# Kernel optimization log

Hardware: AMD Instinct MI355X
Metric: run time of the kernel (lower is better)

Reference implementation:

```python
import jax, jax.numpy as jnp
import numpy as np

B, T, C, HS = 16, 2048, 2048, 256  # batch, seq (=BLOCK_SIZE), N_EMBD, head_size


def setup_inputs() -> dict:
    key = jax.random.key(0)
    k0, k1, k2, k3 = jax.random.split(key, 4)
    token_embd = jax.random.normal(k0, (B, T, C), dtype=jnp.float32)
    # nn.Linear(C, HS, bias=False); store as [C, HS] so projection is x @ W
    scale = 1.0 / np.sqrt(C)
    Wk = jax.random.normal(k1, (C, HS), dtype=jnp.float32) * scale
    Wq = jax.random.normal(k2, (C, HS), dtype=jnp.float32) * scale
    Wv = jax.random.normal(k3, (C, HS), dtype=jnp.float32) * scale
    return {"token_embd": token_embd, "Wk": Wk, "Wq": Wq, "Wv": Wv}


def reference(token_embd, Wk, Wq, Wv):
    Bc, Tc, Cc = token_embd.shape
    k = token_embd @ Wk  # [B,T,HS]
    q = token_embd @ Wq  # [B,T,HS]
    v = token_embd @ Wv  # [B,T,HS]
    # NOTE faithful quirks of the source: k @ q^T (not q @ k^T) and
    # MULTIPLY by sqrt(C) where C = N_EMBD.
    weights = jnp.einsum("bih,bjh->bij", k, q) * (Cc ** 0.5)  # [B,T,T]
    # causal mask: tril==0 (upper triangle, j>i) -> -inf
    i = jnp.arange(Tc)[:, None]
    j = jnp.arange(Tc)[None, :]
    weights = jnp.where(j > i, -jnp.inf, weights)
    # softmax over dim=1 (rows / first T axis), as in the source
    weights = jax.nn.softmax(weights, axis=1)
    # dropout p=0.0 / eval mode -> identity
    output = jnp.einsum("bij,bjh->bih", weights, v)  # [B,T,HS]
    return output
```

## Files before the change

kernel.cpp:

```cpp
#include <hip/hip_runtime.h>
#include <math.h>

#define Bn 16
#define Tn 2048
#define Cn 2048
#define HSn 256
#define SCALE 45.254833995939045f
#define NEG_BIG (-1e30f)
#define NT 16
#define NPAIR 136
#define WN 524288

typedef __attribute__((ext_vector_type(8))) short bf16x8;
typedef __attribute__((ext_vector_type(4))) float f32x4;
typedef unsigned short u16;
typedef unsigned int u32;

__device__ __forceinline__ u16 bf16_rn(float f) {
    u32 u = __float_as_uint(f);
    u += 0x7fffu + ((u >> 16) & 1u);
    return (u16)(u >> 16);
}
__device__ __forceinline__ float bf16_rn_f(float f) {
    return __uint_as_float((u32)bf16_rn(f) << 16);
}

#define GLOAD_LDS16(gp, lp)                                                      \
    __builtin_amdgcn_global_load_lds(                                            \
        (const __attribute__((address_space(1))) unsigned int*)(gp),             \
        (__attribute__((address_space(3))) unsigned int*)(lp), 16, 0, 0)

#define WAITV0_LG0 asm volatile("s_waitcnt vmcnt(0) lgkmcnt(0)" ::: "memory")
#define WAITV2_LG0 asm volatile("s_waitcnt vmcnt(2) lgkmcnt(0)" ::: "memory")
#define WAITLG0    asm volatile("s_waitcnt lgkmcnt(0)" ::: "memory")
#define BARRIER    __builtin_amdgcn_s_barrier()

__global__ __launch_bounds__(256) void split_w_kernel(
    const float* __restrict__ Wk, const float* __restrict__ Wq,
    const float* __restrict__ Wv, u16* __restrict__ Wt)
{
    const int n = threadIdx.x, k = blockIdx.x, mat = blockIdx.y;
    const float* src = (mat == 0) ? Wk : (mat == 1) ? Wq : Wv;
    const float f = src[(long)k * HSn + n];
    const u32 u = __float_as_uint(f);
    const u16 hb = (u16)(u >> 16);
    const float fh = __uint_as_float(u & 0xffff0000u);
    const u16 lb = bf16_rn(f - fh);
    u16* base = Wt + (long)mat * 2 * WN;
    base[(long)n * Cn + k] = hb;
    base[WN + (long)n * Cn + k] = lb;
}

__global__ __launch_bounds__(512, 2) void projm_fused_kernel(
    const float* __restrict__ X, const u16* __restrict__ Wt,
    u16* __restrict__ Khi, u16* __restrict__ Klo,
    u16* __restrict__ Qhi, u16* __restrict__ Qlo, u16* __restrict__ VbfT)
{
    __shared__ u16 Ahi[4096], Alo[4096];
    __shared__ u16 Bbuf[20480];

    const int tid = threadIdx.x, l = tid & 63, w = tid >> 6;
    const int wm = w & 3, wn = w >> 2;
    const int m0 = blockIdx.x * 128, n0 = blockIdx.y * 128;

    int xoff[2], aoff[2];
    #pragma unroll
    for (int p = 0; p < 2; ++p) {
        const int idx4 = p * 512 + tid;
        const int row  = idx4 >> 3;
        const int kk4  = (idx4 & 7) * 4;
        xoff[p] = (m0 + row) * Cn + kk4;
        aoff[p] = (row >> 4) * 512 + (((row & 15) | ((kk4 >> 3) << 4)) * 8) + (kk4 & 7);
    }

    int wgoff[5];
    const int lbase = w * 5 * 512;
    #pragma unroll
    for (int j = 0; j < 5; ++j) {
        const int g    = w * 5 + j;
        const int half = g >> 3;
        const int cc   = g & 7;
        const int nrow = n0 + cc * 16 + (l & 15);
        wgoff[j] = half * WN + nrow * Cn + ((l >> 4) << 3);
    }

    f32x4 accK[2][4], accQ[2][4], accV[2][4];
    #pragma unroll
    for (int mt = 0; mt < 2; ++mt)
        #pragma unroll
        for (int nt = 0; nt < 4; ++nt)
            #pragma unroll
            for (int r = 0; r < 4; ++r) {
                accK[mt][nt][r] = 0.f; accQ[mt][nt][r] = 0.f; accV[mt][nt][r] = 0.f;
            }

    float4 xA[2], xB[2];

    auto convert_write = [&](const float4 (&xr)[2]) {
        #pragma unroll
        for (int p = 0; p < 2; ++p) {
            const float xf[4] = {xr[p].x, xr[p].y, xr[p].z, xr[p].w};
            ushort4 h4, l4;
            #pragma unroll
            for (int c = 0; c < 4; ++c) {
                const u32 u = __float_as_uint(xf[c]);
                ((u16*)&h4)[c] = (u16)(u >> 16);
                const float fh = __uint_as_float(u & 0xffff0000u);
                ((u16*)&l4)[c] = bf16_rn(xf[c] - fh);
            }
            *(ushort4*)(Ahi + aoff[p]) = h4;
            *(ushort4*)(Alo + aoff[p]) = l4;
        }
    };

    auto mfma_all = [&]() {
        bf16x8 ah[2], al[2];
        #pragma unroll
        for (int mt = 0; mt < 2; ++mt) {
            ah[mt] = *(const bf16x8*)(Ahi + (wm * 2 + mt) * 512 + l * 8);
            al[mt] = *(const bf16x8*)(Alo + (wm * 2 + mt) * 512 + l * 8);
        }
        {
            bf16x8 bh[4], bl[4];
            #pragma unroll
            for (int nt = 0; nt < 4; ++nt) {
                bh[nt] = *(const bf16x8*)(Bbuf + (0 * 8 + wn * 4 + nt) * 512 + l * 8);
                bl[nt] = *(const bf16x8*)(Bbuf + (1 * 8 + wn * 4 + nt) * 512 + l * 8);
            }
            #pragma unroll
            for (int mt = 0; mt < 2; ++mt)
                #pragma unroll
                for (int nt = 0; nt < 4; ++nt) {
                    accK[mt][nt] = __builtin_amdgcn_mfma_f32_16x16x32_bf16(ah[mt], bh[nt], accK[mt][nt], 0, 0, 0);
                    accK[mt][nt] = __builtin_amdgcn_mfma_f32_16x16x32_bf16(ah[mt], bl[nt], accK[mt][nt], 0, 0, 0);
                    accK[mt][nt] = __builtin_amdgcn_mfma_f32_16x16x32_bf16(al[mt], bh[nt], accK[mt][nt], 0, 0, 0);
                }
        }
        {
            bf16x8 bh[4], bl[4];
            #pragma unroll
            for (int nt = 0; nt < 4; ++nt) {
                bh[nt] = *(const bf16x8*)(Bbuf + (2 * 8 + wn * 4 + nt) * 512 + l * 8);
                bl[nt] = *(const bf16x8*)(Bbuf + (3 * 8 + wn * 4 + nt) * 512 + l * 8);
            }
            #pragma unroll
            for (int mt = 0; mt < 2; ++mt)
                #pragma unroll
                for (int nt = 0; nt < 4; ++nt) {
                    accQ[mt][nt] = __builtin_amdgcn_mfma_f32_16x16x32_bf16(ah[mt], bh[nt], accQ[mt][nt], 0, 0, 0);
                    accQ[mt][nt] = __builtin_amdgcn_mfma_f32_16x16x32_bf16(ah[mt], bl[nt], accQ[mt][nt], 0, 0, 0);
                    accQ[mt][nt] = __builtin_amdgcn_mfma_f32_16x16x32_bf16(al[mt], bh[nt], accQ[mt][nt], 0, 0, 0);
                }
        }
        {
            bf16x8 bh[4];
            #pragma unroll
            for (int nt = 0; nt < 4; ++nt)
                bh[nt] = *(const bf16x8*)(Bbuf + (4 * 8 + wn * 4 + nt) * 512 + l * 8);
            #pragma unroll
            for (int mt = 0; mt < 2; ++mt)
                #pragma unroll
                for (int nt = 0; nt < 4; ++nt)
                    accV[mt][nt] = __builtin_amdgcn_mfma_f32_16x16x32_bf16(ah[mt], bh[nt], accV[mt][nt], 0, 0, 0);
        }
    };

    xA[0] = *(const float4*)(X + xoff[0]);
    xA[1] = *(const float4*)(X + xoff[1]);

    #pragma unroll 1
    for (int k0 = 0; k0 < Cn; k0 += 64) {
        #pragma unroll
        for (int j = 0; j < 5; ++j)
            GLOAD_LDS16(Wt + wgoff[j] + k0, Bbuf + lbase + j * 512);
        __builtin_amdgcn_sched_barrier(0);
        xB[0] = *(const float4*)(X + xoff[0] + k0 + 32);
        xB[1] = *(const float4*)(X + xoff[1] + k0 + 32);
        convert_write(xA);
        WAITV2_LG0;
        BARRIER;
        mfma_all();
        WAITLG0;
        BARRIER;
        #pragma unroll
        for (int j = 0; j < 5; ++j)
            GLOAD_LDS16(Wt + wgoff[j] + k0 + 32, Bbuf + lbase + j * 512);
        __builtin_amdgcn_sched_barrier(0);
        const int kn = (k0 + 64 < Cn) ? k0 + 64 : 0;
        xA[0] = *(const float4*)(X + xoff[0] + kn);
        xA[1] = *(const float4*)(X + xoff[1] + kn);
        convert_write(xB);
        WAITV2_LG0;
        BARRIER;
        mfma_all();
        WAITLG0;
        BARRIER;
    }

    const int quad = (l >> 4) * 4, col = l & 15;
    u16* Vlds = Bbuf;
    #pragma unroll
    for (int mt = 0; mt < 2; ++mt)
        #pragma unroll
        for (int nt = 0; nt < 4; ++nt)
            #pragma unroll
            for (int r = 0; r < 4; ++r) {
                const long i = m0 + wm * 32 + mt * 16 + quad + r;
                const int  j = n0 + wn * 64 + nt * 16 + col;
                {
                    const float f = accK[mt][nt][r];
                    const u32 u = __float_as_uint(f);
                    Khi[i * HSn + j] = (u16)(u >> 16);
                    const float fh = __uint_as_float(u & 0xffff0000u);
                    Klo[i * HSn + j] = bf16_rn(f - fh);
                }
                {
                    const float f = accQ[mt][nt][r];
                    const u32 u = __float_as_uint(f);
                    Qhi[i * HSn + j] = (u16)(u >> 16);
                    const float fh = __uint_as_float(u & 0xffff0000u);
                    Qlo[i * HSn + j] = bf16_rn(f - fh);
                }
                Vlds[(wm * 32 + mt * 16 + quad + r) * 128 + wn * 64 + nt * 16 + col]
                    = bf16_rn(accV[mt][nt][r]);
            }
    __syncthreads();
    {
        const int bidx = m0 >> 11, jb = m0 & (Tn - 1);
        #pragma unroll
        for (int hh = 0; hh < 4; ++hh) {
            const int hl = hh * 32 + (tid >> 4);
            const int h  = n0 + hl;
            const int jl = (tid & 15) * 8;
            union { uint4 v; u16 s[8]; } pk;
            #pragma unroll
            for (int e = 0; e < 8; ++e) pk.s[e] = Vlds[(jl + e) * 128 + hl];
            *(uint4*)(VbfT + ((long)bidx * HSn + h) * Tn + jb + jl) = pk.v;
        }
    }
}

__device__ __forceinline__ void score_tile_mfma(
    const u16* __restrict__ Khi, const u16* __restrict__ Klo,
    const u16* __restrict__ Qhi, const u16* __restrict__ Qlo,
    long base, int i0, int j0,
    u16* Ab0, u16* Bb0, u16* Ab1, u16* Bb1,
    f32x4 (&acc)[4][4], int tid)
{
    const int l = tid & 63, w = tid >> 6;
    const int wm = w & 1, wn = w >> 1;
    const int lrow = l & 15, lk8 = (l >> 4) << 3;

    #pragma unroll
    for (int a = 0; a < 4; ++a)
        #pragma unroll
        for (int bb = 0; bb < 4; ++bb)
            #pragma unroll
            for (int r = 0; r < 4; ++r) acc[a][bb][r] = 0.f;

    const u16* hiP = wn ? Qhi : Khi;
    const u16* loP = wn ? Qlo : Klo;
    const int  t0  = wn ? j0 : i0;
    long rowoff[4];
    #pragma unroll
    for (int m2 = 0; m2 < 4; ++m2) {
        const int mt = (w & 1) * 4 + m2;
        rowoff[m2] = base + (long)(t0 + mt * 16 + lrow) * HSn + lk8;
    }
    u16* dst0 = (wn ? Bb0 : Ab0) + (w & 1) * 8 * 512;
    u16* dst1 = (wn ? Bb1 : Ab1) + (w & 1) * 8 * 512;

    auto stage = [&](int h0, u16* dw) {
        #pragma unroll
        for (int q = 0; q < 8; ++q) {
            const u16* sp = (q & 1) ? loP : hiP;
            GLOAD_LDS16(sp + rowoff[q >> 1] + h0, dw + q * 512);
        }
    };
    auto step = [&](const u16* Ab, const u16* Bb) {
        bf16x8 bh[4], bl[4];
        #pragma unroll
        for (int nt = 0; nt < 4; ++nt) {
            const int c2 = (wn * 4 + nt) * 2;
            bh[nt] = *(const bf16x8*)(Bb + (c2    ) * 512 + l * 8);
            bl[nt] = *(const bf16x8*)(Bb + (c2 + 1) * 512 + l * 8);
        }
        #pragma unroll
        for (int mt = 0; mt < 4; ++mt) {
            const int c2 = (wm * 4 + mt) * 2;
            const bf16x8 ah = *(const bf16x8*)(Ab + (c2    ) * 512 + l * 8);
            const bf16x8 al = *(const bf16x8*)(Ab + (c2 + 1) * 512 + l * 8);
            #pragma unroll
            for (int nt = 0; nt < 4; ++nt) {
                acc[mt][nt] = __builtin_amdgcn_mfma_f32_16x16x32_bf16(ah, bh[nt], acc[mt][nt], 0, 0, 0);
                acc[mt][nt] = __builtin_amdgcn_mfma_f32_16x16x32_bf16(ah, bl[nt], acc[mt][nt], 0, 0, 0);
                acc[mt][nt] = __builtin_amdgcn_mfma_f32_16x16x32_bf16(al, bh[nt], acc[mt][nt], 0, 0, 0);
            }
        }
    };

    stage(0, dst0);
    WAITV0_LG0;
    BARRIER;
    #pragma unroll 1
    for (int ks = 0; ks < 8; ks += 2) {
        stage((ks + 1) * 32, dst1);
        step(Ab0, Bb0);
        WAITV0_LG0;
        BARRIER;
        if (ks + 2 < 8) stage((ks + 2) * 32, dst0);
        step(Ab1, Bb1);
        WAITV0_LG0;
        BARRIER;
    }
}

__device__ __forceinline__ void pair_from_p(int p, int& it, int& jt) {
    it = (int)((sqrtf(8.f * (float)p + 1.f) - 1.f) * 0.5f);
    while ((it + 1) * (it + 2) / 2 <= p) ++it;
    while (it * (it + 1) / 2 > p) --it;
    jt = p - it * (it + 1) / 2;
}

__global__ __launch_bounds__(256) void stats1_kernel(
    const u16* __restrict__ Khi, const u16* __restrict__ Klo,
    const u16* __restrict__ Qhi, const u16* __restrict__ Qlo,
    u16* __restrict__ Pm, u16* __restrict__ Pd)
{
    __shared__ u16 s_lds[32768];
    __shared__ float redm[2][128], redd[2][128];

    const int tid = threadIdx.x, l = tid & 63, w = tid >> 6;
    const int wm = w & 1, wn = w >> 1;
    const int b = blockIdx.y;
    int it, jt; pair_from_p(blockIdx.x, it, jt);
    const long base = (long)b * Tn * HSn;

    f32x4 acc[4][4];
    score_tile_mfma(Khi, Klo, Qhi, Qlo, base, it * 128, jt * 128,
                    s_lds, s_lds + 8192, s_lds + 16384, s_lds + 24576, acc, tid);

    const int rquad = (l >> 4) * 4, col = l & 15;
    #pragma unroll
    for (int nt = 0; nt < 4; ++nt) {
        const int j = jt * 128 + wn * 64 + nt * 16 + col;
        float m = NEG_BIG;
        #pragma unroll
        for (int mt = 0; mt < 4; ++mt)
            #pragma unroll
            for (int r = 0; r < 4; ++r) {
                const int i = it * 128 + wm * 64 + mt * 16 + rquad + r;
                const float sv = (i >= j) ? acc[mt][nt][r] * SCALE : NEG_BIG;
                acc[mt][nt][r] = sv;
                m = fmaxf(m, sv);
            }
        m = fmaxf(m, __shfl_xor(m, 16));
        m = fmaxf(m, __shfl_xor(m, 32));
        float d = 0.f;
        #pragma unroll
        for (int mt = 0; mt < 4; ++mt)
            #pragma unroll
            for (int r = 0; r < 4; ++r)
                d += __expf(acc[mt][nt][r] - m);
        d += __shfl_xor(d, 16);
        d += __shfl_xor(d, 32);
        if (l < 16) {
            redm[wm][wn * 64 + nt * 16 + l] = m;
            redd[wm][wn * 64 + nt * 16 + l] = d;
        }
    }
    __syncthreads();
    if (tid < 128) {
        const float m0 = redm[0][tid], m1 = redm[1][tid];
        const float d0 = redd[0][tid], d1 = redd[1][tid];
        const float M = fmaxf(m0, m1);
        float D = d0 * __expf(m0 - M) + d1 * __expf(m1 - M);
        const float Mb = bf16_rn_f(M);
        D *= __expf(M - Mb);
        const long idx = ((long)b * NPAIR + blockIdx.x) * 128 + tid;
        Pm[idx] = (u16)(__float_as_uint(Mb) >> 16);
        Pd[idx] = bf16_rn(D);
    }
}

__global__ __launch_bounds__(128) void stats2_kernel(
    const u16* __restrict__ Pm, const u16* __restrict__ Pd,
    float* __restrict__ Ms, float* __restrict__ Rd)
{
    const int b = blockIdx.y, jt = blockIdx.x, jl = threadIdx.x;
    float M = NEG_BIG, D = 0.f;
    for (int it = jt; it < NT; ++it) {
        const int p = it * (it + 1) / 2 + jt;
        const long idx = ((long)b * NPAIR + p) * 128 + jl;
        const float m = __uint_as_float((u32)Pm[idx] << 16);
        const float d = __uint_as_float((u32)Pd[idx] << 16);
        const float Mn = fmaxf(M, m);
        D = D * __expf(M - Mn) + d * __expf(m - Mn);
        M = Mn;
    }
    Ms[(long)b * Tn + jt * 128 + jl] = M;
    Rd[(long)b * Tn + jt * 128 + jl] = 1.f / D;
}

__global__ __launch_bounds__(256) void out_kernel(
    const u16* __restrict__ Khi, const u16* __restrict__ Klo,
    const u16* __restrict__ Qhi, const u16* __restrict__ Qlo,
    const u16* __restrict__ VbfT, const float* __restrict__ Ms,
    const float* __restrict__ Rd, float* __restrict__ Out)
{
    __shared__ u16 u_lds[33792];
    u16* Pf    = u_lds;
    u16* Vfrag = u_lds + 17408;

    const int tid = threadIdx.x, l = tid & 63, w = tid >> 6;
    const int wm = w & 1, wn = w >> 1;
    const int lrow = l & 15, lk8 = (l >> 4) << 3;
    const int b = blockIdx.y;
    int it, jt; pair_from_p(blockIdx.x, it, jt);
    const long base = (long)b * Tn * HSn;

    f32x4 acc[4][4];
    score_tile_mfma(Khi, Klo, Qhi, Qlo, base, it * 128, jt * 128,
                    u_lds, u_lds + 8192, u_lds + 16384, u_lds + 24576, acc, tid);

    auto stage_v = [&](int ph) {
        #pragma unroll
        for (int q = 0; q < 8; ++q) {
            const int hh = ph * 128 + q * 16 + lrow;
            const long ga = ((long)b * HSn + hh) * Tn + jt * 128 + w * 32 + lk8;
            GLOAD_LDS16(VbfT + ga, Vfrag + (w * 8 + q) * 512);
        }
    };

    stage_v(0);

    const int rquad = (l >> 4) * 4, col = l & 15;
    float mj[4], rj[4];
    #pragma unroll
    for (int nt = 0; nt < 4; ++nt) {
        const int j = jt * 128 + wn * 64 + nt * 16 + col;
        mj[nt] = Ms[(long)b * Tn + j];
        rj[nt] = Rd[(long)b * Tn + j];
    }
    #pragma unroll
    for (int nt = 0; nt < 4; ++nt) {
        const int j = jt * 128 + wn * 64 + nt * 16 + col;
        #pragma unroll
        for (int mt = 0; mt < 4; ++mt)
            #pragma unroll
            for (int r = 0; r < 4; ++r) {
                const int i = it * 128 + wm * 64 + mt * 16 + rquad + r;
                const float pv = (i >= j)
                    ? __expf(acc[mt][nt][r] * SCALE - mj[nt]) * rj[nt] : 0.f;
                Pf[(wm * 64 + mt * 16 + rquad + r) * 136 + wn * 64 + nt * 16 + col]
                    = bf16_rn(pv);
            }
    }

    auto pv_store = [&](int ph) {
        f32x4 o[4][4];
        #pragma unroll
        for (int a = 0; a < 4; ++a)
            #pragma unroll
            for (int bb = 0; bb < 4; ++bb)
                #pragma unroll
                for (int r = 0; r < 4; ++r) o[a][bb][r] = 0.f;
        #pragma unroll
        for (int kj = 0; kj < 4; ++kj) {
            bf16x8 aP[4];
            #pragma unroll
            for (int mt = 0; mt < 4; ++mt)
                aP[mt] = *(const bf16x8*)(Pf + (wm * 64 + mt * 16 + lrow) * 136 + kj * 32 + lk8);
            #pragma unroll
            for (int nt = 0; nt < 4; ++nt) {
                const bf16x8 bV = *(const bf16x8*)(Vfrag + (kj * 8 + wn * 4 + nt) * 512 + l * 8);
                #pragma unroll
                for (int mt = 0; mt < 4; ++mt)
                    o[mt][nt] = __builtin_amdgcn_mfma_f32_16x16x32_bf16(aP[mt], bV, o[mt][nt], 0, 0, 0);
            }
        }
        #pragma unroll
        for (int mt = 0; mt < 4; ++mt)
            #pragma unroll
            for (int nt = 0; nt < 4; ++nt)
                #pragma unroll
                for (int r = 0; r < 4; ++r) {
                    const int i = it * 128 + wm * 64 + mt * 16 + rquad + r;
                    const int h = ph * 128 + wn * 64 + nt * 16 + col;
                    atomicAdd(&Out[((long)b * Tn + i) * HSn + h], o[mt][nt][r]);
                }
    };

    __syncthreads();
    pv_store(0);
    __syncthreads();
    stage_v(1);
    __syncthreads();
    pv_store(1);
}

extern "C" void kernel_launch(void* const* d_in, const int* in_sizes, int n_in,
                              void* d_out, int out_size, void* d_ws, size_t ws_size,
                              hipStream_t stream) {
    const float* X  = (const float*)d_in[0];
    const float* Wk = (const float*)d_in[1];
    const float* Wq = (const float*)d_in[2];
    const float* Wv = (const float*)d_in[3];

    const long nE = (long)Bn * Tn * HSn;
    u16* Khi = (u16*)d_ws;
    u16* Klo = Khi + nE;
    u16* Qhi = Khi + 2 * nE;
    u16* Qlo = Khi + 3 * nE;
    u16* VbfT = Khi + 4 * nE;
    u16* Wt  = Khi + 5 * nE;
    u16* Pm  = Wt + 6L * WN;
    u16* Pd  = Pm + (long)Bn * NPAIR * 128;
    float* Ms = (float*)(Pd + (long)Bn * NPAIR * 128);
    float* Rd = Ms + (long)Bn * Tn;

    split_w_kernel<<<dim3(Cn, 3), 256, 0, stream>>>(Wk, Wq, Wv, Wt);
    projm_fused_kernel<<<dim3((Bn * Tn) / 128, HSn / 128), 512, 0, stream>>>(
        X, Wt, Khi, Klo, Qhi, Qlo, VbfT);
    stats1_kernel<<<dim3(NPAIR, Bn), 256, 0, stream>>>(Khi, Klo, Qhi, Qlo, Pm, Pd);
    stats2_kernel<<<dim3(NT, Bn), 128, 0, stream>>>(Pm, Pd, Ms, Rd);
    hipMemsetAsync(d_out, 0, (size_t)out_size * sizeof(float), stream);
    out_kernel<<<dim3(NPAIR, Bn), 256, 0, stream>>>(Khi, Klo, Qhi, Qlo, VbfT, Ms, Rd,
                                                    (float*)d_out);
}
```

Baseline: 1.005 ms.

## Double-buffer projection LDS, single-buffer score tile, pipeline V staging in PV

The projection kernel gets ping-pong LDS buffers for the A and B tiles, so the next slice's loads and conversion overlap the current MFMA work and one barrier pair per half-step goes away. The score-tile helper drops its double buffering to a single buffer with a full wait each step, which shrinks LDS use in the stats and PV kernels, presumably to allow more resident blocks. The PV kernel splits the head dimension into four 64-wide phases and issues the next V slice before the atomic stores, so staging overlaps the output writes. The trade-off is less latency hiding in the score GEMM and more LDS use in the projection kernel.

```diff
diff --git a/kernel.cpp b/kernel.cpp
--- a/kernel.cpp
+++ b/kernel.cpp
@@ -30,10 +30,11 @@
         (const __attribute__((address_space(1))) unsigned int*)(gp),             \
         (__attribute__((address_space(3))) unsigned int*)(lp), 16, 0, 0)
 
-#define WAITV0_LG0 asm volatile("s_waitcnt vmcnt(0) lgkmcnt(0)" ::: "memory")
-#define WAITV2_LG0 asm volatile("s_waitcnt vmcnt(2) lgkmcnt(0)" ::: "memory")
-#define WAITLG0    asm volatile("s_waitcnt lgkmcnt(0)" ::: "memory")
-#define BARRIER    __builtin_amdgcn_s_barrier()
+#define WAITV0_LG0  asm volatile("s_waitcnt vmcnt(0) lgkmcnt(0)" ::: "memory")
+#define WAITV2_LG0  asm volatile("s_waitcnt vmcnt(2) lgkmcnt(0)" ::: "memory")
+#define WAITV32_LG0 asm volatile("s_waitcnt vmcnt(32) lgkmcnt(0)" ::: "memory")
+#define WAITLG0     asm volatile("s_waitcnt lgkmcnt(0)" ::: "memory")
+#define BARRIER     __builtin_amdgcn_s_barrier()
 
 __global__ __launch_bounds__(256) void split_w_kernel(
     const float* __restrict__ Wk, const float* __restrict__ Wq,
@@ -56,8 +57,8 @@
     u16* __restrict__ Khi, u16* __restrict__ Klo,
     u16* __restrict__ Qhi, u16* __restrict__ Qlo, u16* __restrict__ VbfT)
 {
-    __shared__ u16 Ahi[4096], Alo[4096];
-    __shared__ u16 Bbuf[20480];
+    __shared__ u16 Ahi0[4096], Alo0[4096], Ahi1[4096], Alo1[4096];
+    __shared__ u16 Bb0[20480], Bb1[20480];
 
     const int tid = threadIdx.x, l = tid & 63, w = tid >> 6;
     const int wm = w & 3, wn = w >> 2;
@@ -96,7 +97,7 @@
 
     float4 xA[2], xB[2];
 
-    auto convert_write = [&](const float4 (&xr)[2]) {
+    auto convert_write = [&](const float4 (&xr)[2], u16* Ah, u16* Al) {
         #pragma unroll
         for (int p = 0; p < 2; ++p) {
             const float xf[4] = {xr[p].x, xr[p].y, xr[p].z, xr[p].w};
@@ -108,24 +109,24 @@
                 const float fh = __uint_as_float(u & 0xffff0000u);
                 ((u16*)&l4)[c] = bf16_rn(xf[c] - fh);
             }
-            *(ushort4*)(Ahi + aoff[p]) = h4;
-            *(ushort4*)(Alo + aoff[p]) = l4;
+            *(ushort4*)(Ah + aoff[p]) = h4;
+            *(ushort4*)(Al + aoff[p]) = l4;
         }
     };
 
-    auto mfma_all = [&]() {
+    auto mfma_all = [&](const u16* Ah, const u16* Al, const u16* Bb) {
         bf16x8 ah[2], al[2];
         #pragma unroll
         for (int mt = 0; mt < 2; ++mt) {
-            ah[mt] = *(const bf16x8*)(Ahi + (wm * 2 + mt) * 512 + l * 8);
-            al[mt] = *(const bf16x8*)(Alo + (wm * 2 + mt) * 512 + l * 8);
+            ah[mt] = *(const bf16x8*)(Ah + (wm * 2 + mt) * 512 + l * 8);
+            al[mt] = *(const bf16x8*)(Al + (wm * 2 + mt) * 512 + l * 8);
         }
         {
             bf16x8 bh[4], bl[4];
             #pragma unroll
             for (int nt = 0; nt < 4; ++nt) {
-                bh[nt] = *(const bf16x8*)(Bbuf + (0 * 8 + wn * 4 + nt) * 512 + l * 8);
-                bl[nt] = *(const bf16x8*)(Bbuf + (1 * 8 + wn * 4 + nt) * 512 + l * 8);
+                bh[nt] = *(const bf16x8*)(Bb + (0 * 8 + wn * 4 + nt) * 512 + l * 8);
+                bl[nt] = *(const bf16x8*)(Bb + (1 * 8 + wn * 4 + nt) * 512 + l * 8);
             }
             #pragma unroll
             for (int mt = 0; mt < 2; ++mt)
@@ -140,8 +141,8 @@
             bf16x8 bh[4], bl[4];
             #pragma unroll
             for (int nt = 0; nt < 4; ++nt) {
-                bh[nt] = *(const bf16x8*)(Bbuf + (2 * 8 + wn * 4 + nt) * 512 + l * 8);
-                bl[nt] = *(const bf16x8*)(Bbuf + (3 * 8 + wn * 4 + nt) * 512 + l * 8);
+                bh[nt] = *(const bf16x8*)(Bb + (2 * 8 + wn * 4 + nt) * 512 + l * 8);
+                bl[nt] = *(const bf16x8*)(Bb + (3 * 8 + wn * 4 + nt) * 512 + l * 8);
             }
             #pragma unroll
             for (int mt = 0; mt < 2; ++mt)
@@ -156,7 +157,7 @@
             bf16x8 bh[4];
             #pragma unroll
             for (int nt = 0; nt < 4; ++nt)
-                bh[nt] = *(const bf16x8*)(Bbuf + (4 * 8 + wn * 4 + nt) * 512 + l * 8);
+                bh[nt] = *(const bf16x8*)(Bb + (4 * 8 + wn * 4 + nt) * 512 + l * 8);
             #pragma unroll
             for (int mt = 0; mt < 2; ++mt)
                 #pragma unroll
@@ -167,38 +168,42 @@
 
     xA[0] = *(const float4*)(X + xoff[0]);
     xA[1] = *(const float4*)(X + xoff[1]);
+    #pragma unroll
+    for (int j = 0; j < 5; ++j)
+        GLOAD_LDS16(Wt + wgoff[j], Bb0 + lbase + j * 512);
+    xB[0] = *(const float4*)(X + xoff[0] + 32);
+    xB[1] = *(const float4*)(X + xoff[1] + 32);
+    convert_write(xA, Ahi0, Alo0);
+    WAITV2_LG0;
+    BARRIER;
 
     #pragma unroll 1
     for (int k0 = 0; k0 < Cn; k0 += 64) {
+        const int kn  = (k0 + 64 < Cn) ? k0 + 64 : 0;
+        const int kn3 = (k0 + 96 < Cn) ? k0 + 96 : 0;
         #pragma unroll
         for (int j = 0; j < 5; ++j)
-            GLOAD_LDS16(Wt + wgoff[j] + k0, Bbuf + lbase + j * 512);
-        __builtin_amdgcn_sched_barrier(0);
-        xB[0] = *(const float4*)(X + xoff[0] + k0 + 32);
-        xB[1] = *(const float4*)(X + xoff[1] + k0 + 32);
-        convert_write(xA);
+            GLOAD_LDS16(Wt + wgoff[j] + k0 + 32, Bb1 + lbase + j * 512);
+        xA[0] = *(const float4*)(X + xoff[0] + kn);
+        xA[1] = *(const float4*)(X + xoff[1] + kn);
+        convert_write(xB, Ahi1, Alo1);
+        mfma_all(Ahi0, Alo0, Bb0);
         WAITV2_LG0;
         BARRIER;
-        mfma_all();
-        WAITLG0;
-        BARRIER;
         #pragma unroll
         for (int j = 0; j < 5; ++j)
-            GLOAD_LDS16(Wt + wgoff[j] + k0 + 32, Bbuf + lbase + j * 512);
-        __builtin_amdgcn_sched_barrier(0);
-        const int kn = (k0 + 64 < Cn) ? k0 + 64 : 0;
-        xA[0] = *(const float4*)(X + xoff[0] + kn);
-        xA[1] = *(const float4*)(X + xoff[1] + kn);
-        convert_write(xB);
+            GLOAD_LDS16(Wt + wgoff[j] + kn, Bb0 + lbase + j * 512);
+        xB[0] = *(const float4*)(X + xoff[0] + kn3);
+        xB[1] = *(const float4*)(X + xoff[1] + kn3);
+        convert_write(xA, Ahi0, Alo0);
+        mfma_all(Ahi1, Alo1, Bb1);
         WAITV2_LG0;
         BARRIER;
-        mfma_all();
-        WAITLG0;
-        BARRIER;
     }
 
     const int quad = (l >> 4) * 4, col = l & 15;
-    u16* Vlds = Bbuf;
+    u16* Vlds = Bb0;
+    __syncthreads();
     #pragma unroll
     for (int mt = 0; mt < 2; ++mt)
         #pragma unroll
@@ -244,7 +249,7 @@
     const u16* __restrict__ Khi, const u16* __restrict__ Klo,
     const u16* __restrict__ Qhi, const u16* __restrict__ Qlo,
     long base, int i0, int j0,
-    u16* Ab0, u16* Bb0, u16* Ab1, u16* Bb1,
+    u16* Ab0, u16* Bb0,
     f32x4 (&acc)[4][4], int tid)
 {
     const int l = tid & 63, w = tid >> 6;
@@ -268,28 +273,29 @@
         rowoff[m2] = base + (long)(t0 + mt * 16 + lrow) * HSn + lk8;
     }
     u16* dst0 = (wn ? Bb0 : Ab0) + (w & 1) * 8 * 512;
-    u16* dst1 = (wn ? Bb1 : Ab1) + (w & 1) * 8 * 512;
-
-    auto stage = [&](int h0, u16* dw) {
+
+    #pragma unroll 1
+    for (int ks = 0; ks < 8; ++ks) {
+        const int h0 = ks * 32;
         #pragma unroll
         for (int q = 0; q < 8; ++q) {
             const u16* sp = (q & 1) ? loP : hiP;
-            GLOAD_LDS16(sp + rowoff[q >> 1] + h0, dw + q * 512);
-        }
-    };
-    auto step = [&](const u16* Ab, const u16* Bb) {
+            GLOAD_LDS16(sp + rowoff[q >> 1] + h0, dst0 + q * 512);
+        }
+        WAITV0_LG0;
+        BARRIER;
         bf16x8 bh[4], bl[4];
         #pragma unroll
         for (int nt = 0; nt < 4; ++nt) {
             const int c2 = (wn * 4 + nt) * 2;
-            bh[nt] = *(const bf16x8*)(Bb + (c2    ) * 512 + l * 8);
-            bl[nt] = *(const bf16x8*)(Bb + (c2 + 1) * 512 + l * 8);
+            bh[nt] = *(const bf16x8*)(Bb0 + (c2    ) * 512 + l * 8);
+            bl[nt] = *(const bf16x8*)(Bb0 + (c2 + 1) * 512 + l * 8);
         }
         #pragma unroll
         for (int mt = 0; mt < 4; ++mt) {
             const int c2 = (wm * 4 + mt) * 2;
-            const bf16x8 ah = *(const bf16x8*)(Ab + (c2    ) * 512 + l * 8);
-            const bf16x8 al = *(const bf16x8*)(Ab + (c2 + 1) * 512 + l * 8);
+            const bf16x8 ah = *(const bf16x8*)(Ab0 + (c2    ) * 512 + l * 8);
+            const bf16x8 al = *(const bf16x8*)(Ab0 + (c2 + 1) * 512 + l * 8);
             #pragma unroll
             for (int nt = 0; nt < 4; ++nt) {
                 acc[mt][nt] = __builtin_amdgcn_mfma_f32_16x16x32_bf16(ah, bh[nt], acc[mt][nt], 0, 0, 0);
@@ -297,20 +303,7 @@
                 acc[mt][nt] = __builtin_amdgcn_mfma_f32_16x16x32_bf16(al, bh[nt], acc[mt][nt], 0, 0, 0);
             }
         }
-    };
-
-    stage(0, dst0);
-    WAITV0_LG0;
-    BARRIER;
-    #pragma unroll 1
-    for (int ks = 0; ks < 8; ks += 2) {
-        stage((ks + 1) * 32, dst1);
-        step(Ab0, Bb0);
-        WAITV0_LG0;
-        BARRIER;
-        if (ks + 2 < 8) stage((ks + 2) * 32, dst0);
-        step(Ab1, Bb1);
-        WAITV0_LG0;
+        WAITLG0;
         BARRIER;
     }
 }
@@ -327,7 +320,7 @@
     const u16* __restrict__ Qhi, const u16* __restrict__ Qlo,
     u16* __restrict__ Pm, u16* __restrict__ Pd)
 {
-    __shared__ u16 s_lds[32768];
+    __shared__ u16 s_lds[16384];
     __shared__ float redm[2][128], redd[2][128];
 
     const int tid = threadIdx.x, l = tid & 63, w = tid >> 6;
@@ -338,7 +331,7 @@
 
     f32x4 acc[4][4];
     score_tile_mfma(Khi, Klo, Qhi, Qlo, base, it * 128, jt * 128,
-                    s_lds, s_lds + 8192, s_lds + 16384, s_lds + 24576, acc, tid);
+                    s_lds, s_lds + 8192, acc, tid);
 
     const int rquad = (l >> 4) * 4, col = l & 15;
     #pragma unroll
@@ -408,7 +401,7 @@
     const u16* __restrict__ VbfT, const float* __restrict__ Ms,
     const float* __restrict__ Rd, float* __restrict__ Out)
 {
-    __shared__ u16 u_lds[33792];
+    __shared__ u16 u_lds[25600];
     u16* Pf    = u_lds;
     u16* Vfrag = u_lds + 17408;
 
@@ -421,14 +414,14 @@
 
     f32x4 acc[4][4];
     score_tile_mfma(Khi, Klo, Qhi, Qlo, base, it * 128, jt * 128,
-                    u_lds, u_lds + 8192, u_lds + 16384, u_lds + 24576, acc, tid);
+                    u_lds, u_lds + 8192, acc, tid);
 
     auto stage_v = [&](int ph) {
         #pragma unroll
-        for (int q = 0; q < 8; ++q) {
-            const int hh = ph * 128 + q * 16 + lrow;
+        for (int q = 0; q < 4; ++q) {
+            const int hh = ph * 64 + q * 16 + lrow;
             const long ga = ((long)b * HSn + hh) * Tn + jt * 128 + w * 32 + lk8;
-            GLOAD_LDS16(VbfT + ga, Vfrag + (w * 8 + q) * 512);
+            GLOAD_LDS16(VbfT + ga, Vfrag + (w * 4 + q) * 512);
         }
     };
 
@@ -457,12 +450,15 @@
             }
     }
 
-    auto pv_store = [&](int ph) {
-        f32x4 o[4][4];
+    __syncthreads();
+
+    #pragma unroll 1
+    for (int ph = 0; ph < 4; ++ph) {
+        f32x4 o[4][2];
         #pragma unroll
         for (int a = 0; a < 4; ++a)
             #pragma unroll
-            for (int bb = 0; bb < 4; ++bb)
+            for (int bb = 0; bb < 2; ++bb)
                 #pragma unroll
                 for (int r = 0; r < 4; ++r) o[a][bb][r] = 0.f;
         #pragma unroll
@@ -472,31 +468,32 @@
             for (int mt = 0; mt < 4; ++mt)
                 aP[mt] = *(const bf16x8*)(Pf + (wm * 64 + mt * 16 + lrow) * 136 + kj * 32 + lk8);
             #pragma unroll
-            for (int nt = 0; nt < 4; ++nt) {
-                const bf16x8 bV = *(const bf16x8*)(Vfrag + (kj * 8 + wn * 4 + nt) * 512 + l * 8);
+            for (int nt = 0; nt < 2; ++nt) {
+                const bf16x8 bV = *(const bf16x8*)(Vfrag + (kj * 4 + wn * 2 + nt) * 512 + l * 8);
                 #pragma unroll
                 for (int mt = 0; mt < 4; ++mt)
                     o[mt][nt] = __builtin_amdgcn_mfma_f32_16x16x32_bf16(aP[mt], bV, o[mt][nt], 0, 0, 0);
             }
         }
+        WAITLG0;
+        BARRIER;
+        if (ph < 3) stage_v(ph + 1);
+        __builtin_amdgcn_sched_barrier(0);
         #pragma unroll
         for (int mt = 0; mt < 4; ++mt)
             #pragma unroll
-            for (int nt = 0; nt < 4; ++nt)
+            for (int nt = 0; nt < 2; ++nt)
                 #pragma unroll
                 for (int r = 0; r < 4; ++r) {
                     const int i = it * 128 + wm * 64 + mt * 16 + rquad + r;
-                    const int h = ph * 128 + wn * 64 + nt * 16 + col;
+                    const int h = ph * 64 + wn * 32 + nt * 16 + col;
                     atomicAdd(&Out[((long)b * Tn + i) * HSn + h], o[mt][nt][r]);
                 }
-    };
-
-    __syncthreads();
-    pv_store(0);
-    __syncthreads();
-    stage_v(1);
-    __syncthreads();
-    pv_store(1);
+        if (ph < 3) {
+            WAITV32_LG0;
+            BARRIER;
+        }
+    }
 }
 
 extern "C" void kernel_launch(void* const* d_in, const int* in_sizes, int n_in,
```

Result: faster. 975.4 us (-2.9%).
